# Kernel tuning notes

Measured on AMD Instinct MI355X. Metric: run time of the kernel, lower is better.

The kernel has to match this reference:

```python
import jax, jax.numpy as jnp
import numpy as np

B, T, C, HS = 8, 4096, 1024, 64  # batch, seq, n_embd, head_size


def setup_inputs() -> dict:
    key = jax.random.key(0)
    kx, kk, kq, kv = jax.random.split(key, 4)
    x = jax.random.normal(kx, (B, T, C), dtype=jnp.float32)
    # bias-free linear weights, stored as [in, out] like flax kernels
    s = 1.0 / np.sqrt(C)
    Wk = jax.random.normal(kk, (C, HS), dtype=jnp.float32) * s
    Wq = jax.random.normal(kq, (C, HS), dtype=jnp.float32) * s
    Wv = jax.random.normal(kv, (C, HS), dtype=jnp.float32) * s
    return {"x": x, "Wk": Wk, "Wq": Wq, "Wv": Wv}


def reference(x, Wk, Wq, Wv):
    # x: [B, T, C]
    Tq = x.shape[1]
    Cdim = x.shape[2]
    k = jnp.einsum('btc,ch->bth', x, Wk)  # [B,T,HS]
    q = jnp.einsum('btc,ch->bth', x, Wq)
    v = jnp.einsum('btc,ch->bth', x, Wv)
    # NOTE: original scales by C**-0.5 (full embed dim), not head_size**-0.5
    scale = Cdim ** (-0.5)
    wei = jnp.einsum('bth,bsh->bts', q, k) * scale  # [B,T,T]
    causal = jnp.tril(jnp.ones((Tq, Tq), dtype=bool))
    wei = jnp.where(causal, wei, -jnp.inf)
    wei = jax.nn.softmax(wei, axis=-1)
    out = jnp.einsum('bts,bsh->bth', wei, v)  # [B,T,HS]
    return out
```

## Files before the change

kernel.cpp:

```cpp
#include <hip/hip_runtime.h>
#include <hip/hip_bf16.h>


typedef __attribute__((ext_vector_type(8))) short short8;
typedef __attribute__((ext_vector_type(8))) unsigned short ushort8;
typedef __attribute__((ext_vector_type(4))) float f32x4;
typedef __attribute__((ext_vector_type(16))) float f32x16;
typedef __attribute__((ext_vector_type(4))) unsigned int u32x4;

#define NB 8
#define NT 4096
#define NC 1024
#define NH 64

__device__ __forceinline__ unsigned short f2bf(float f) {
    unsigned int u = __builtin_bit_cast(unsigned int, f);
    u += 0x7fffu + ((u >> 16) & 1u);
    return (unsigned short)(u >> 16);
}

__device__ __forceinline__ float bf2f(unsigned short u) {
    return __builtin_bit_cast(float, (unsigned int)u << 16);
}

__device__ __forceinline__ unsigned cvt_pk_bf16(float lo, float hi) {
    unsigned r;
    asm("v_cvt_pk_bf16_f32 %0, %1, %2" : "=v"(r) : "v"(lo), "v"(hi));
    return r;
}

#define GLOAD16(gp, lp)                                                        \
    __builtin_amdgcn_global_load_lds(                                          \
        (const __attribute__((address_space(1))) void*)(gp),                   \
        (__attribute__((address_space(3))) void*)(lp), 16, 0, 0)

__global__ __launch_bounds__(256) void wprep_kernel(
    const float* __restrict__ Wk, const float* __restrict__ Wq,
    const float* __restrict__ Wv, unsigned short* __restrict__ Wt)
{
    int n = blockIdx.x;
    int which = n >> 6, h = n & 63;
    const float* W = (which == 0) ? Wk : (which == 1) ? Wq : Wv;
    for (int c = threadIdx.x; c < NC; c += 256)
        Wt[(size_t)n * NC + c] = f2bf(W[(size_t)c * NH + h]);
}

__global__ __launch_bounds__(256, 2) void proj_kernel(
    const float* __restrict__ x, const unsigned short* __restrict__ Wt,
    unsigned short* __restrict__ qws, unsigned short* __restrict__ kws,
    unsigned short* __restrict__ vtws)
{
    __shared__ char lds[4][20480];

    const int lane = threadIdx.x & 63;
    const int wave = threadIdx.x >> 6;
    const int l15 = lane & 15;
    const int kg = lane >> 4;
    const int m0 = blockIdx.x * 64;

    const int agS = (lane & 7) ^ (lane >> 3);
    const float* aSrc[2];
#pragma unroll
    for (int j = 0; j < 2; ++j) {
        int i = wave * 2 + j;
        int r = 8 * i + (lane >> 3);
        aSrc[j] = x + (size_t)(m0 + r) * NC + agS * 4;
    }
    const int bgS = (lane & 3) ^ ((lane >> 2) & 3);
    const unsigned short* bSrc[3];
#pragma unroll
    for (int j = 0; j < 3; ++j) {
        int u = wave * 3 + j;
        int r = 16 * u + (lane >> 2);
        bSrc[j] = Wt + (size_t)r * NC + bgS * 8;
    }

    f32x4 acc[12];
#pragma unroll
    for (int i = 0; i < 12; ++i) acc[i] = f32x4{0.f, 0.f, 0.f, 0.f};

#define STAGE_CHUNK(c)                                                         \
    do {                                                                       \
        char* base_ = lds[(c) & 3];                                            \
        _Pragma("unroll")                                                      \
        for (int j = 0; j < 2; ++j)                                            \
            GLOAD16(aSrc[j] + (c) * 32, base_ + (wave * 2 + j) * 1024);        \
        _Pragma("unroll")                                                      \
        for (int j = 0; j < 3; ++j)                                            \
            GLOAD16(bSrc[j] + (c) * 32, base_ + 8192 + (wave * 3 + j) * 1024); \
    } while (0)

    STAGE_CHUNK(0);
    STAGE_CHUNK(1);

    for (int kc = 0; kc < 32; ++kc) {
        if (kc < 30) {
            STAGE_CHUNK(kc + 2);
            asm volatile("s_waitcnt vmcnt(10)" ::: "memory");
        } else if (kc == 30) {
            asm volatile("s_waitcnt vmcnt(5)" ::: "memory");
        } else {
            asm volatile("s_waitcnt vmcnt(0)" ::: "memory");
        }
        __builtin_amdgcn_sched_barrier(0);
        __builtin_amdgcn_s_barrier();

        const char* Ab = lds[kc & 3];
        const char* Bb = lds[kc & 3] + 8192;
        {
            const int r = wave * 16 + l15;
            const int g0 = kg * 2;
            f32x4 a0 = *(const f32x4*)(Ab + r * 128 + ((g0 ^ (r & 7)) * 16));
            f32x4 a1 = *(const f32x4*)(Ab + r * 128 + (((g0 + 1) ^ (r & 7)) * 16));
            short8 a;
            a[0] = (short)f2bf(a0[0]); a[1] = (short)f2bf(a0[1]);
            a[2] = (short)f2bf(a0[2]); a[3] = (short)f2bf(a0[3]);
            a[4] = (short)f2bf(a1[0]); a[5] = (short)f2bf(a1[1]);
            a[6] = (short)f2bf(a1[2]); a[7] = (short)f2bf(a1[3]);
#pragma unroll
            for (int nt = 0; nt < 12; ++nt) {
                int rb = nt * 16 + l15;
                short8 bfrag = *(const short8*)(
                    Bb + rb * 64 + ((kg ^ (rb & 3)) * 16));
                acc[nt] = __builtin_amdgcn_mfma_f32_16x16x32_bf16(a, bfrag, acc[nt], 0, 0, 0);
            }
        }
    }
#undef STAGE_CHUNK

    const float cs = 0.04508422f;
    const int crow0 = m0 + wave * 16 + (kg << 2);
#pragma unroll
    for (int nt = 0; nt < 12; ++nt) {
        int n = nt * 16 + l15;
        int which = n >> 6;
        int h = n & 63;
#pragma unroll
        for (int r = 0; r < 4; ++r) {
            int gm = crow0 + r;
            float av = acc[nt][r];
            if (which == 1) av *= cs;
            unsigned short v = f2bf(av);
            if (which == 0) {
                kws[(size_t)gm * NH + h] = v;
            } else if (which == 1) {
                qws[(size_t)gm * NH + h] = v;
            } else {
                int bb = gm >> 12, tt = gm & 4095;
                vtws[((size_t)(bb * NH + h)) * NT + tt] = v;
            }
        }
    }
}

__global__ __launch_bounds__(256, 4) void flash_kernel(
    const unsigned short* __restrict__ qws, const unsigned short* __restrict__ kws,
    const unsigned short* __restrict__ vtws,
    unsigned short* __restrict__ opart, float* __restrict__ mlpart)
{
    __shared__ unsigned short Kbuf[2][64 * 64];
    __shared__ unsigned short Vbuf[2][64 * 64];

    const int id = blockIdx.x;
    const int g = id >> 5;
    const int p = (id >> 3) & 3;
    const int b = id & 7;
    const int a = g & 7, m = g >> 3;
    const int qt = (m == 0) ? 31 - a : (m == 1) ? 16 + a : (m == 2) ? 15 - a : a;
    const int n = 2 * qt + 2;
    const int len = (n + 3) >> 2;
    const int k0 = p * len;
    const int k1 = (k0 + len < n) ? (k0 + len) : n;

    float* mlp = mlpart + (size_t)id * 256;
    unsigned short* op = opart + (size_t)id * 8192;

    const int lane = threadIdx.x & 63;
    const int wave = threadIdx.x >> 6;
    const int l31 = lane & 31;
    const int hi = lane >> 5;
    const int rsw = lane & 7;

    const int sg = (lane & 7) ^ (lane >> 3);
    const unsigned short* kSrc[2];
    const unsigned short* vSrc[2];
#pragma unroll
    for (int j = 0; j < 2; ++j) {
        int r = 16 * wave + 8 * j + (lane >> 3);
        kSrc[j] = kws + ((size_t)(b * NT) + r) * NH + sg * 8;
        vSrc[j] = vtws + ((size_t)(b * NH + r)) * NT + sg * 8;
    }

    const int qmin = qt * 128 + wave * 32;
    short8 qf[4];
    {
        const char* qp = (const char*)(qws + ((size_t)(b * NT) + qmin + l31) * NH);
#pragma unroll
        for (int s = 0; s < 4; ++s)
            qf[s] = *(const short8*)(qp + s * 32 + hi * 16);
    }

    f32x16 o0, o1;
#pragma unroll
    for (int i = 0; i < 16; ++i) { o0[i] = 0.f; o1[i] = 0.f; }
    float m_r = -INFINITY;
    float l_r = 0.f;

    const int kst = (k0 < n) ? k0 : (n - 1);
#pragma unroll
    for (int j = 0; j < 2; ++j) {
        int i = 2 * wave + j;
        GLOAD16(kSrc[j] + (size_t)kst * 64 * NH, (char*)Kbuf[0] + i * 1024);
        GLOAD16(vSrc[j] + (size_t)kst * 64,      (char*)Vbuf[0] + i * 1024);
    }
    __syncthreads();

    int cur = 0;
    for (int kv = k0; kv < k1; ++kv) {
        if (kv + 1 < k1) {
#pragma unroll
            for (int j = 0; j < 2; ++j) {
                int i = 2 * wave + j;
                GLOAD16(kSrc[j] + (size_t)(kv + 1) * 64 * NH,
                        (char*)Kbuf[cur ^ 1] + i * 1024);
                GLOAD16(vSrc[j] + (size_t)(kv + 1) * 64,
                        (char*)Vbuf[cur ^ 1] + i * 1024);
            }
        }

        const char* Kb = (const char*)Kbuf[cur];
        const char* Vb = (const char*)Vbuf[cur];

        f32x16 st0, st1;
#pragma unroll
        for (int i = 0; i < 16; ++i) { st0[i] = 0.f; st1[i] = 0.f; }
        __builtin_amdgcn_s_setprio(1);
#pragma unroll
        for (int s = 0; s < 4; ++s) {
            int gl = s * 2 + hi;
            short8 ka = *(const short8*)(Kb + l31 * 128 + ((gl ^ rsw) << 4));
            short8 kb = *(const short8*)(Kb + (32 + l31) * 128 + ((gl ^ rsw) << 4));
            st0 = __builtin_amdgcn_mfma_f32_32x32x16_bf16(ka, qf[s], st0, 0, 0, 0);
            st1 = __builtin_amdgcn_mfma_f32_32x32x16_bf16(kb, qf[s], st1, 0, 0, 0);
        }
        __builtin_amdgcn_s_setprio(0);

        const int kb0 = kv * 64;
        if (kb0 + 63 > qmin) {
            const int qg = qmin + l31;
#pragma unroll
            for (int r = 0; r < 16; ++r) {
                int key = kb0 + (r & 3) + 8 * (r >> 2) + 4 * hi;
                if (key > qg) st0[r] = -1e30f;
                if (key + 32 > qg) st1[r] = -1e30f;
            }
        }

        float lmax;
        {
            float a0 = fmaxf(fmaxf(st0[0], st0[1]), st0[2]);
            float a1 = fmaxf(fmaxf(st0[3], st0[4]), st0[5]);
            float a2 = fmaxf(fmaxf(st0[6], st0[7]), st0[8]);
            float a3 = fmaxf(fmaxf(st0[9], st0[10]), st0[11]);
            float a4 = fmaxf(fmaxf(st0[12], st0[13]), st0[14]);
            float a5 = fmaxf(fmaxf(st0[15], st1[0]), st1[1]);
            float a6 = fmaxf(fmaxf(st1[2], st1[3]), st1[4]);
            float a7 = fmaxf(fmaxf(st1[5], st1[6]), st1[7]);
            float a8 = fmaxf(fmaxf(st1[8], st1[9]), st1[10]);
            float a9 = fmaxf(fmaxf(st1[11], st1[12]), st1[13]);
            float aa = fmaxf(st1[14], st1[15]);
            float b0 = fmaxf(fmaxf(a0, a1), a2);
            float b1 = fmaxf(fmaxf(a3, a4), a5);
            float b2 = fmaxf(fmaxf(a6, a7), a8);
            float b3 = fmaxf(a9, aa);
            lmax = fmaxf(fmaxf(b0, b1), fmaxf(b2, b3));
        }

        if (!__all(lmax <= m_r + 8.0f)) {
            float pmax = fmaxf(lmax, __shfl_xor(lmax, 32));
            float mn = fmaxf(m_r, pmax);
            float alpha = __builtin_amdgcn_exp2f(m_r - mn);
            m_r = mn;
            l_r *= alpha;
#pragma unroll
            for (int r = 0; r < 16; ++r) { o0[r] *= alpha; o1[r] *= alpha; }
        }

        float psum = 0.f;
#pragma unroll
        for (int r = 0; r < 16; ++r) {
            st0[r] = __builtin_amdgcn_exp2f(st0[r] - m_r);
            st1[r] = __builtin_amdgcn_exp2f(st1[r] - m_r);
            psum += st0[r] + st1[r];
        }
        l_r += psum;

        __builtin_amdgcn_s_setprio(1);
#pragma unroll
        for (int kt = 0; kt < 2; ++kt) {
            const f32x16& st = kt ? st1 : st0;
            unsigned w0 = cvt_pk_bf16(st[0], st[1]),   w1 = cvt_pk_bf16(st[2], st[3]);
            unsigned w2 = cvt_pk_bf16(st[4], st[5]),   w3 = cvt_pk_bf16(st[6], st[7]);
            unsigned w4 = cvt_pk_bf16(st[8], st[9]),   w5 = cvt_pk_bf16(st[10], st[11]);
            unsigned w6 = cvt_pk_bf16(st[12], st[13]), w7 = cvt_pk_bf16(st[14], st[15]);
            asm("v_permlane32_swap_b32 %0, %1" : "+v"(w0), "+v"(w2));
            asm("v_permlane32_swap_b32 %0, %1" : "+v"(w1), "+v"(w3));
            asm("v_permlane32_swap_b32 %0, %1" : "+v"(w4), "+v"(w6));
            asm("v_permlane32_swap_b32 %0, %1" : "+v"(w5), "+v"(w7));
            u32x4 wA, wB;
            wA[0] = w0; wA[1] = w1; wA[2] = w2; wA[3] = w3;
            wB[0] = w4; wB[1] = w5; wB[2] = w6; wB[3] = w7;
            short8 pfA = __builtin_bit_cast(short8, wA);
            short8 pfB = __builtin_bit_cast(short8, wB);
#pragma unroll
            for (int w = 0; w < 2; ++w) {
                short8 pf = w ? pfB : pfA;
                int gv = (kt * 2 + w) * 2 + hi;
                short8 va = *(const short8*)(Vb + l31 * 128 + ((gv ^ rsw) << 4));
                short8 vb = *(const short8*)(Vb + (32 + l31) * 128 + ((gv ^ rsw) << 4));
                o0 = __builtin_amdgcn_mfma_f32_32x32x16_bf16(va, pf, o0, 0, 0, 0);
                o1 = __builtin_amdgcn_mfma_f32_32x32x16_bf16(vb, pf, o1, 0, 0, 0);
            }
        }
        __builtin_amdgcn_s_setprio(0);

        __syncthreads();
        cur ^= 1;
    }

    float lt = l_r + __shfl_xor(l_r, 32);
    const int row = wave * 32 + l31;
    unsigned short* orow = op + row * 64;
#pragma unroll
    for (int blk = 0; blk < 4; ++blk) {
        uint2 t0, t1;
        t0.x = cvt_pk_bf16(o0[blk * 4 + 0], o0[blk * 4 + 1]);
        t0.y = cvt_pk_bf16(o0[blk * 4 + 2], o0[blk * 4 + 3]);
        t1.x = cvt_pk_bf16(o1[blk * 4 + 0], o1[blk * 4 + 1]);
        t1.y = cvt_pk_bf16(o1[blk * 4 + 2], o1[blk * 4 + 3]);
        *(uint2*)(orow + 8 * blk + 4 * hi) = t0;
        *(uint2*)(orow + 32 + 8 * blk + 4 * hi) = t1;
    }
    if (hi == 0) {
        mlp[row] = m_r;
        mlp[128 + row] = lt;
    }
}

__global__ __launch_bounds__(256) void combine_kernel(
    const unsigned short* __restrict__ opart, const float* __restrict__ mlpart,
    float* __restrict__ out)
{
    const int cid = blockIdx.x;
    const int qt = cid >> 3, b = cid & 7;
    int g;
    if (qt >= 24) g = 31 - qt;
    else if (qt >= 16) g = 8 + (qt - 16);
    else if (qt >= 8) g = 16 + (15 - qt);
    else g = 24 + qt;
    const int pidb = g * 32 + b;

    const float* ml[4];
    const ushort8* ov[4];
#pragma unroll
    for (int p = 0; p < 4; ++p) {
        ml[p] = mlpart + (size_t)(pidb + p * 8) * 256;
        ov[p] = (const ushort8*)(opart + (size_t)(pidb + p * 8) * 8192);
    }

#pragma unroll
    for (int i = 0; i < 4; ++i) {
        int gidx = threadIdx.x + i * 256;
        int row = gidx >> 3;
        float m0 = ml[0][row], m1 = ml[1][row], m2 = ml[2][row], m3 = ml[3][row];
        float ms = fmaxf(fmaxf(m0, m1), fmaxf(m2, m3));
        float e0 = __builtin_amdgcn_exp2f(m0 - ms);
        float e1 = __builtin_amdgcn_exp2f(m1 - ms);
        float e2 = __builtin_amdgcn_exp2f(m2 - ms);
        float e3 = __builtin_amdgcn_exp2f(m3 - ms);
        float den = e0 * ml[0][128 + row] + e1 * ml[1][128 + row] +
                    e2 * ml[2][128 + row] + e3 * ml[3][128 + row];
        float dinv = __builtin_amdgcn_rcpf(den);
        ushort8 a0 = ov[0][gidx], a1 = ov[1][gidx], a2 = ov[2][gidx], a3 = ov[3][gidx];
        float r[8];
#pragma unroll
        for (int c = 0; c < 8; ++c)
            r[c] = (e0 * bf2f(a0[c]) + e1 * bf2f(a1[c]) +
                    e2 * bf2f(a2[c]) + e3 * bf2f(a3[c])) * dinv;
        float* gp = out + ((size_t)(b * NT) + qt * 128 + row) * NH + (gidx & 7) * 8;
        f32x4 w0, w1;
        w0[0] = r[0]; w0[1] = r[1]; w0[2] = r[2]; w0[3] = r[3];
        w1[0] = r[4]; w1[1] = r[5]; w1[2] = r[6]; w1[3] = r[7];
        *(f32x4*)(gp) = w0;
        *(f32x4*)(gp + 4) = w1;
    }
}

extern "C" void kernel_launch(void* const* d_in, const int* in_sizes, int n_in,
                              void* d_out, int out_size, void* d_ws, size_t ws_size,
                              hipStream_t stream) {
    const float* x  = (const float*)d_in[0];
    const float* Wk = (const float*)d_in[1];
    const float* Wq = (const float*)d_in[2];
    const float* Wv = (const float*)d_in[3];
    float* out = (float*)d_out;

    unsigned short* ws   = (unsigned short*)d_ws;
    const size_t qkv_elems = (size_t)NB * NT * NH;
    unsigned short* qws  = ws;
    unsigned short* kws  = qws + qkv_elems;
    unsigned short* vtws = kws + qkv_elems;
    unsigned short* Wt   = vtws + qkv_elems;
    unsigned short* opart = Wt + (size_t)192 * NC;
    float* mlpart = (float*)(opart + (size_t)1024 * 8192);

    wprep_kernel<<<dim3(192), dim3(256), 0, stream>>>(Wk, Wq, Wv, Wt);
    proj_kernel<<<dim3(512), dim3(256), 0, stream>>>(x, Wt, qws, kws, vtws);
    flash_kernel<<<dim3(1024), dim3(256), 0, stream>>>(qws, kws, vtws, opart, mlpart);
    combine_kernel<<<dim3(256), dim3(256), 0, stream>>>(opart, mlpart, out);
}
```

Measured before the change: 73.40 us.

## Split causal KV range five ways with new tile-to-block mapping

The flash kernel now splits each query tile's causal KV range into five partitions instead of four. It launches 1280 blocks with a launch bound of five blocks per CU, and a new permutation assigns query tiles to blocks within each partition. Blocks whose KV slice is empty write neutral partials (zero output, -inf max, zero sum) and exit. The combine kernel is updated to merge five partials through the matching inverse permutation. The softmax row-sum is also reassociated into a tree to shorten the dependency chain. The aim is better load balance and occupancy across the causal triangle, at the cost of extra partial traffic, more combine work and tighter register limits.

```diff
diff --git a/kernel.cpp b/kernel.cpp
--- a/kernel.cpp
+++ b/kernel.cpp
@@ -153,7 +153,7 @@
     }
 }
 
-__global__ __launch_bounds__(256, 4) void flash_kernel(
+__global__ __launch_bounds__(256, 5) void flash_kernel(
     const unsigned short* __restrict__ qws, const unsigned short* __restrict__ kws,
     const unsigned short* __restrict__ vtws,
     unsigned short* __restrict__ opart, float* __restrict__ mlpart)
@@ -162,18 +162,31 @@
     __shared__ unsigned short Vbuf[2][64 * 64];
 
     const int id = blockIdx.x;
-    const int g = id >> 5;
-    const int p = (id >> 3) & 3;
-    const int b = id & 7;
-    const int a = g & 7, m = g >> 3;
-    const int qt = (m == 0) ? 31 - a : (m == 1) ? 16 + a : (m == 2) ? 15 - a : a;
+    const int p = id >> 8;
+    const int cu = id & 255;
+    const int b = cu & 7;
+    const int h = cu >> 3;
+    int qt;
+    if (p == 0) qt = h;
+    else if (p == 1) qt = 31 - h;
+    else if (p == 2) qt = (h + 16) & 31;
+    else if (p == 3) qt = (15 - h) & 31;
+    else qt = (13 * h + 7) & 31;
     const int n = 2 * qt + 2;
-    const int len = (n + 3) >> 2;
+    const int len = (n + 4) / 5;
     const int k0 = p * len;
     const int k1 = (k0 + len < n) ? (k0 + len) : n;
 
     float* mlp = mlpart + (size_t)id * 256;
     unsigned short* op = opart + (size_t)id * 8192;
+
+    if (k0 >= k1) {
+        uint4 z; z.x = 0; z.y = 0; z.z = 0; z.w = 0;
+        uint4* o4 = (uint4*)op;
+        for (int i = threadIdx.x; i < 1024; i += 256) o4[i] = z;
+        mlp[threadIdx.x] = (threadIdx.x < 128) ? -INFINITY : 0.f;
+        return;
+    }
 
     const int lane = threadIdx.x & 63;
     const int wave = threadIdx.x >> 6;
@@ -206,12 +219,11 @@
     float m_r = -INFINITY;
     float l_r = 0.f;
 
-    const int kst = (k0 < n) ? k0 : (n - 1);
 #pragma unroll
     for (int j = 0; j < 2; ++j) {
         int i = 2 * wave + j;
-        GLOAD16(kSrc[j] + (size_t)kst * 64 * NH, (char*)Kbuf[0] + i * 1024);
-        GLOAD16(vSrc[j] + (size_t)kst * 64,      (char*)Vbuf[0] + i * 1024);
+        GLOAD16(kSrc[j] + (size_t)k0 * 64 * NH, (char*)Kbuf[0] + i * 1024);
+        GLOAD16(vSrc[j] + (size_t)k0 * 64,      (char*)Vbuf[0] + i * 1024);
     }
     __syncthreads();
 
@@ -286,14 +298,22 @@
             for (int r = 0; r < 16; ++r) { o0[r] *= alpha; o1[r] *= alpha; }
         }
 
-        float psum = 0.f;
 #pragma unroll
         for (int r = 0; r < 16; ++r) {
             st0[r] = __builtin_amdgcn_exp2f(st0[r] - m_r);
             st1[r] = __builtin_amdgcn_exp2f(st1[r] - m_r);
-            psum += st0[r] + st1[r];
-        }
-        l_r += psum;
+        }
+        {
+            float q0 = (st0[0] + st0[1]) + (st0[2] + st0[3]);
+            float q1 = (st0[4] + st0[5]) + (st0[6] + st0[7]);
+            float q2 = (st0[8] + st0[9]) + (st0[10] + st0[11]);
+            float q3 = (st0[12] + st0[13]) + (st0[14] + st0[15]);
+            float q4 = (st1[0] + st1[1]) + (st1[2] + st1[3]);
+            float q5 = (st1[4] + st1[5]) + (st1[6] + st1[7]);
+            float q6 = (st1[8] + st1[9]) + (st1[10] + st1[11]);
+            float q7 = (st1[12] + st1[13]) + (st1[14] + st1[15]);
+            l_r += ((q0 + q1) + (q2 + q3)) + ((q4 + q5) + (q6 + q7));
+        }
 
         __builtin_amdgcn_s_setprio(1);
 #pragma unroll
@@ -353,40 +373,45 @@
 {
     const int cid = blockIdx.x;
     const int qt = cid >> 3, b = cid & 7;
-    int g;
-    if (qt >= 24) g = 31 - qt;
-    else if (qt >= 16) g = 8 + (qt - 16);
-    else if (qt >= 8) g = 16 + (15 - qt);
-    else g = 24 + qt;
-    const int pidb = g * 32 + b;
-
-    const float* ml[4];
-    const ushort8* ov[4];
-#pragma unroll
-    for (int p = 0; p < 4; ++p) {
-        ml[p] = mlpart + (size_t)(pidb + p * 8) * 256;
-        ov[p] = (const ushort8*)(opart + (size_t)(pidb + p * 8) * 8192);
+    int hp[5];
+    hp[0] = qt;
+    hp[1] = 31 - qt;
+    hp[2] = (qt + 16) & 31;
+    hp[3] = (15 - qt) & 31;
+    hp[4] = (5 * qt - 3) & 31;
+
+    const float* ml[5];
+    const ushort8* ov[5];
+#pragma unroll
+    for (int p = 0; p < 5; ++p) {
+        int pid = p * 256 + (hp[p] << 3) + b;
+        ml[p] = mlpart + (size_t)pid * 256;
+        ov[p] = (const ushort8*)(opart + (size_t)pid * 8192);
     }
 
 #pragma unroll
     for (int i = 0; i < 4; ++i) {
         int gidx = threadIdx.x + i * 256;
         int row = gidx >> 3;
-        float m0 = ml[0][row], m1 = ml[1][row], m2 = ml[2][row], m3 = ml[3][row];
-        float ms = fmaxf(fmaxf(m0, m1), fmaxf(m2, m3));
+        float m0 = ml[0][row], m1 = ml[1][row], m2 = ml[2][row];
+        float m3 = ml[3][row], m4 = ml[4][row];
+        float ms = fmaxf(fmaxf(fmaxf(m0, m1), fmaxf(m2, m3)), m4);
         float e0 = __builtin_amdgcn_exp2f(m0 - ms);
         float e1 = __builtin_amdgcn_exp2f(m1 - ms);
         float e2 = __builtin_amdgcn_exp2f(m2 - ms);
         float e3 = __builtin_amdgcn_exp2f(m3 - ms);
+        float e4 = __builtin_amdgcn_exp2f(m4 - ms);
         float den = e0 * ml[0][128 + row] + e1 * ml[1][128 + row] +
-                    e2 * ml[2][128 + row] + e3 * ml[3][128 + row];
+                    e2 * ml[2][128 + row] + e3 * ml[3][128 + row] +
+                    e4 * ml[4][128 + row];
         float dinv = __builtin_amdgcn_rcpf(den);
-        ushort8 a0 = ov[0][gidx], a1 = ov[1][gidx], a2 = ov[2][gidx], a3 = ov[3][gidx];
+        ushort8 a0 = ov[0][gidx], a1 = ov[1][gidx], a2 = ov[2][gidx];
+        ushort8 a3 = ov[3][gidx], a4 = ov[4][gidx];
         float r[8];
 #pragma unroll
         for (int c = 0; c < 8; ++c)
-            r[c] = (e0 * bf2f(a0[c]) + e1 * bf2f(a1[c]) +
-                    e2 * bf2f(a2[c]) + e3 * bf2f(a3[c])) * dinv;
+            r[c] = (e0 * bf2f(a0[c]) + e1 * bf2f(a1[c]) + e2 * bf2f(a2[c]) +
+                    e3 * bf2f(a3[c]) + e4 * bf2f(a4[c])) * dinv;
         float* gp = out + ((size_t)(b * NT) + qt * 128 + row) * NH + (gidx & 7) * 8;
         f32x4 w0, w1;
         w0[0] = r[0]; w0[1] = r[1]; w0[2] = r[2]; w0[3] = r[3];
@@ -412,10 +437,10 @@
     unsigned short* vtws = kws + qkv_elems;
     unsigned short* Wt   = vtws + qkv_elems;
     unsigned short* opart = Wt + (size_t)192 * NC;
-    float* mlpart = (float*)(opart + (size_t)1024 * 8192);
+    float* mlpart = (float*)(opart + (size_t)1280 * 8192);
 
     wprep_kernel<<<dim3(192), dim3(256), 0, stream>>>(Wk, Wq, Wv, Wt);
     proj_kernel<<<dim3(512), dim3(256), 0, stream>>>(x, Wt, qws, kws, vtws);
-    flash_kernel<<<dim3(1024), dim3(256), 0, stream>>>(qws, kws, vtws, opart, mlpart);
+    flash_kernel<<<dim3(1280), dim3(256), 0, stream>>>(qws, kws, vtws, opart, mlpart);
     combine_kernel<<<dim3(256), dim3(256), 0, stream>>>(opart, mlpart, out);
 }
```

Result: slower. 103.8 us (+41.5%).
